# Performance work log

Measured on AMD Instinct MI355X. Metric: run time of the kernel, lower is better.

Reference implementation:

```python
import jax, jax.numpy as jnp
import numpy as np

GROUPS = 16
GROUP_SIZE = 16
K = 3
KK = K * K
BN_EPS = 1e-5


def setup_inputs() -> dict:
    key = jax.random.key(0)
    ks = jax.random.split(key, 6)
    B, C, H, W = 16, 256, 56, 56
    mid = C // 4  # rd_ratio = 4
    x = jax.random.normal(ks[0], (B, C, H, W), dtype=jnp.float32)
    w1 = jax.random.normal(ks[1], (mid, C), dtype=jnp.float32) * (1.0 / np.sqrt(C))
    bn_gamma = jnp.ones((mid,), dtype=jnp.float32)
    bn_beta = jnp.zeros((mid,), dtype=jnp.float32)
    bn_mean = jax.random.normal(ks[2], (mid,), dtype=jnp.float32) * 0.1
    bn_var = jax.random.uniform(ks[3], (mid,), dtype=jnp.float32, minval=0.5, maxval=1.5)
    w2 = jax.random.normal(ks[4], (KK * GROUPS, mid), dtype=jnp.float32) * (1.0 / np.sqrt(mid))
    b2 = jax.random.normal(ks[5], (KK * GROUPS,), dtype=jnp.float32) * 0.01
    return {"x": x, "w1": w1, "bn_gamma": bn_gamma, "bn_beta": bn_beta,
            "bn_mean": bn_mean, "bn_var": bn_var, "w2": w2, "b2": b2}


def reference(x, w1, bn_gamma, bn_beta, bn_mean, bn_var, w2, b2):
    B, C, H, W = x.shape
    # conv1: 1x1 conv + BatchNorm (eval) + ReLU
    t = jnp.einsum('bchw,oc->bohw', x, w1)
    scale = bn_gamma / jnp.sqrt(bn_var + BN_EPS)
    t = t * scale[None, :, None, None] + (bn_beta - bn_mean * scale)[None, :, None, None]
    t = jax.nn.relu(t)
    # conv2: 1x1 conv producing per-pixel kernels (B, KK*groups, H, W)
    weight = jnp.einsum('bchw,oc->bohw', t, w2) + b2[None, :, None, None]
    weight = weight.reshape(B, GROUPS, 1, KK, H, W)
    # unfold: extract 3x3 patches (pad=1, stride=1), kernel positions row-major
    xp = jnp.pad(x, ((0, 0), (0, 0), (1, 1), (1, 1)))
    patches = jnp.stack(
        [xp[:, :, i:i + H, j:j + W] for i in range(K) for j in range(K)],
        axis=2)  # (B, C, KK, H, W), matches torch unfold's (c*KK + kk) layout
    patches = patches.reshape(B, GROUPS, GROUP_SIZE, KK, H, W)
    out = (weight * patches).sum(axis=3).reshape(B, C, H, W)
    return out
```

## Files before the change

### kernel.cpp

```cpp
#include <hip/hip_runtime.h>


#define Cn    256
#define MID   64
#define Hn    56
#define Wn    56
#define HW    3136
#define Bn    16
#define NPIX  (Bn * HW)
#define CHW   (Cn * HW)
#define NKK   9
#define NG    16
#define GSZ   16
#define PXT   64
#define BN_EPS 1e-5f

#define GLOAD_LDS(src, dst, sz)                                                        \
  __builtin_amdgcn_global_load_lds(                                                    \
      (const __attribute__((address_space(1))) void*)(src),                            \
      (__attribute__((address_space(3))) void*)(dst), (sz), 0, 0)

__global__ __launch_bounds__(256) void prep_kernel(
    const float* __restrict__ w1,
    const float* __restrict__ gamma,
    const float* __restrict__ beta,
    const float* __restrict__ mean,
    const float* __restrict__ var,
    float* __restrict__ w1f,
    float* __restrict__ bias1) {
  int idx = blockIdx.x * 256 + threadIdx.x;
  if (idx < MID * Cn) {
    int c = idx >> 6;
    int o = idx & 63;
    float scale = gamma[o] / sqrtf(var[o] + BN_EPS);
    w1f[idx] = w1[o * Cn + c] * scale;
  } else if (idx < MID * Cn + MID) {
    int o = idx - MID * Cn;
    float scale = gamma[o] / sqrtf(var[o] + BN_EPS);
    bias1[o] = beta[o] - mean[o] * scale;
  }
}

__global__ __launch_bounds__(256) void fused_kernel(
    const float* __restrict__ x,
    const float* __restrict__ w1f,
    const float* __restrict__ bias1,
    const float* __restrict__ w2,
    const float* __restrict__ b2,
    float* __restrict__ out) {
  __shared__ float lt[MID][PXT];
  __shared__ __align__(16) float uni[9216];

  const int tid = threadIdx.x;
  const int px  = tid & 63;
  const int wvv = tid >> 6;
  const int wv  = __builtin_amdgcn_readfirstlane(wvv);

  const int px0 = blockIdx.x * PXT;
  const int b   = px0 / HW;
  const int hw0 = px0 - b * HW;
  const float* xb = x + (size_t)b * CHW + hw0;

  {
#pragma unroll
    for (int j = 0; j < 4; ++j) {
      const int c = (wv << 2) + j;
      GLOAD_LDS(xb + (size_t)c * HW + px, &uni[c * 64], 4);
    }
    GLOAD_LDS(w1f + (wv << 8) + (px << 2), &uni[2048 + (wv << 8)], 16);
  }
  __syncthreads();

  float acc[16];
#pragma unroll
  for (int j = 0; j < 16; ++j) acc[j] = 0.0f;

  for (int k = 0; k < 16; ++k) {
    const int cur = k & 1;
    if (k < 15) {
      const int nb = cur ^ 1;
      const int kb = k + 1;
#pragma unroll
      for (int j = 0; j < 4; ++j) {
        const int c = (wv << 2) + j;
        GLOAD_LDS(xb + (size_t)(kb * 16 + c) * HW + px, &uni[nb * 1024 + c * 64], 4);
      }
      GLOAD_LDS(w1f + kb * 1024 + (wv << 8) + (px << 2),
                &uni[2048 + nb * 1024 + (wv << 8)], 16);
    }
    const float* lx = &uni[cur * 1024];
    const float* lw = &uni[2048 + cur * 1024 + (wv << 4)];
#pragma unroll
    for (int c = 0; c < 16; ++c) {
      const float xv = lx[(c << 6) + px];
      const float4 w40 = *(const float4*)(lw + (c << 6) + 0);
      const float4 w41 = *(const float4*)(lw + (c << 6) + 4);
      const float4 w42 = *(const float4*)(lw + (c << 6) + 8);
      const float4 w43 = *(const float4*)(lw + (c << 6) + 12);
      acc[0]  = fmaf(xv, w40.x, acc[0]);
      acc[1]  = fmaf(xv, w40.y, acc[1]);
      acc[2]  = fmaf(xv, w40.z, acc[2]);
      acc[3]  = fmaf(xv, w40.w, acc[3]);
      acc[4]  = fmaf(xv, w41.x, acc[4]);
      acc[5]  = fmaf(xv, w41.y, acc[5]);
      acc[6]  = fmaf(xv, w41.z, acc[6]);
      acc[7]  = fmaf(xv, w41.w, acc[7]);
      acc[8]  = fmaf(xv, w42.x, acc[8]);
      acc[9]  = fmaf(xv, w42.y, acc[9]);
      acc[10] = fmaf(xv, w42.z, acc[10]);
      acc[11] = fmaf(xv, w42.w, acc[11]);
      acc[12] = fmaf(xv, w43.x, acc[12]);
      acc[13] = fmaf(xv, w43.y, acc[13]);
      acc[14] = fmaf(xv, w43.z, acc[14]);
      acc[15] = fmaf(xv, w43.w, acc[15]);
    }
    __syncthreads();
  }

#pragma unroll
  for (int j = 0; j < 16; ++j) {
    const int o = (wv << 4) + j;
    lt[o][px] = fmaxf(acc[j] + bias1[o], 0.0f);
  }
#pragma unroll
  for (int i = 0; i < 9; ++i) {
    const int r = wv * 9 + i;
    GLOAD_LDS(w2 + ((size_t)r << 8) + (px << 2), &uni[r << 8], 16);
  }
  __syncthreads();

  const int hw = hw0 + px;
  const int h  = hw / Wn;
  const int w  = hw - h * Wn;

  int off[NKK];
  unsigned vmask = 0;
#pragma unroll
  for (int kk = 0; kk < NKK; ++kk) {
    const int di  = kk / 3 - 1;
    const int dj  = kk % 3 - 1;
    const int h2  = h + di;
    const int w2v = w + dj;
    const bool valid = ((unsigned)h2 < (unsigned)Hn) && ((unsigned)w2v < (unsigned)Wn);
    off[kk] = valid ? (h2 * Wn + w2v) : hw;
    vmask |= (valid ? 1u : 0u) << kk;
  }

  const float* xg = x + (size_t)b * CHW;
  float* ob = out + (size_t)b * CHW + hw;

  for (int gi = 0; gi < 4; ++gi) {
    const int g = wv + (gi << 2);
    float a[NKK];
#pragma unroll
    for (int kk = 0; kk < NKK; ++kk) a[kk] = b2[g * NKK + kk];

#pragma unroll 4
    for (int o4 = 0; o4 < MID; o4 += 4) {
      const float t0 = lt[o4 + 0][px];
      const float t1 = lt[o4 + 1][px];
      const float t2 = lt[o4 + 2][px];
      const float t3 = lt[o4 + 3][px];
#pragma unroll
      for (int kk = 0; kk < NKK; ++kk) {
        const float4 w4 = *(const float4*)&uni[((g * NKK + kk) << 6) + o4];
        a[kk] = fmaf(t3, w4.w, fmaf(t2, w4.z, fmaf(t1, w4.y, fmaf(t0, w4.x, a[kk]))));
      }
    }

    float wk[NKK];
#pragma unroll
    for (int kk = 0; kk < NKK; ++kk)
      wk[kk] = ((vmask >> kk) & 1u) ? a[kk] : 0.0f;

    const float* xc0 = xg + (size_t)(g * GSZ) * HW;
#pragma unroll 4
    for (int cc = 0; cc < GSZ; ++cc) {
      const float* xc = xc0 + (size_t)cc * HW;
      float s = 0.0f;
#pragma unroll
      for (int kk = 0; kk < NKK; ++kk)
        s = fmaf(wk[kk], xc[off[kk]], s);
      ob[(size_t)(g * GSZ + cc) * HW] = s;
    }
  }
}

extern "C" void kernel_launch(void* const* d_in, const int* in_sizes, int n_in,
                              void* d_out, int out_size, void* d_ws, size_t ws_size,
                              hipStream_t stream) {
  const float* x     = (const float*)d_in[0];
  const float* w1    = (const float*)d_in[1];
  const float* gamma = (const float*)d_in[2];
  const float* beta  = (const float*)d_in[3];
  const float* mean  = (const float*)d_in[4];
  const float* var   = (const float*)d_in[5];
  const float* w2    = (const float*)d_in[6];
  const float* b2    = (const float*)d_in[7];
  float* out = (float*)d_out;

  char* ws = (char*)d_ws;
  float* w1f   = (float*)ws;
  float* bias1 = (float*)(ws + (size_t)MID * Cn * 4);

  prep_kernel<<<(MID * Cn + MID + 255) / 256, 256, 0, stream>>>(
      w1, gamma, beta, mean, var, w1f, bias1);
  fused_kernel<<<NPIX / PXT, 256, 0, stream>>>(x, w1f, bias1, w2, b2, out);
}
```

Baseline: 197.6 us.

## Split fused kernel into conv1 and per-group-quarter conv2/involution kernels

Result: faster. 176.4 us (-10.7%).

```diff
diff --git a/kernel.cpp b/kernel.cpp
--- a/kernel.cpp
+++ b/kernel.cpp
@@ -41,15 +41,12 @@
   }
 }
 
-__global__ __launch_bounds__(256) void fused_kernel(
+__global__ __launch_bounds__(256) void conv1_kernel(
     const float* __restrict__ x,
     const float* __restrict__ w1f,
     const float* __restrict__ bias1,
-    const float* __restrict__ w2,
-    const float* __restrict__ b2,
-    float* __restrict__ out) {
-  __shared__ float lt[MID][PXT];
-  __shared__ __align__(16) float uni[9216];
+    float* __restrict__ t) {
+  __shared__ __align__(16) float sb[4096];
 
   const int tid = threadIdx.x;
   const int px  = tid & 63;
@@ -61,14 +58,12 @@
   const int hw0 = px0 - b * HW;
   const float* xb = x + (size_t)b * CHW + hw0;
 
-  {
-#pragma unroll
-    for (int j = 0; j < 4; ++j) {
-      const int c = (wv << 2) + j;
-      GLOAD_LDS(xb + (size_t)c * HW + px, &uni[c * 64], 4);
-    }
-    GLOAD_LDS(w1f + (wv << 8) + (px << 2), &uni[2048 + (wv << 8)], 16);
-  }
+#pragma unroll
+  for (int j = 0; j < 4; ++j) {
+    const int c = (wv << 2) + j;
+    GLOAD_LDS(xb + (size_t)c * HW + px, &sb[c * 64], 4);
+  }
+  GLOAD_LDS(w1f + (wv << 8) + (px << 2), &sb[2048 + (wv << 8)], 16);
   __syncthreads();
 
   float acc[16];
@@ -83,13 +78,13 @@
 #pragma unroll
       for (int j = 0; j < 4; ++j) {
         const int c = (wv << 2) + j;
-        GLOAD_LDS(xb + (size_t)(kb * 16 + c) * HW + px, &uni[nb * 1024 + c * 64], 4);
+        GLOAD_LDS(xb + (size_t)(kb * 16 + c) * HW + px, &sb[nb * 1024 + c * 64], 4);
       }
       GLOAD_LDS(w1f + kb * 1024 + (wv << 8) + (px << 2),
-                &uni[2048 + nb * 1024 + (wv << 8)], 16);
+                &sb[2048 + nb * 1024 + (wv << 8)], 16);
     }
-    const float* lx = &uni[cur * 1024];
-    const float* lw = &uni[2048 + cur * 1024 + (wv << 4)];
+    const float* lx = &sb[cur * 1024];
+    const float* lw = &sb[2048 + cur * 1024 + (wv << 4)];
 #pragma unroll
     for (int c = 0; c < 16; ++c) {
       const float xv = lx[(c << 6) + px];
@@ -120,14 +115,60 @@
 #pragma unroll
   for (int j = 0; j < 16; ++j) {
     const int o = (wv << 4) + j;
-    lt[o][px] = fmaxf(acc[j] + bias1[o], 0.0f);
-  }
-#pragma unroll
-  for (int i = 0; i < 9; ++i) {
-    const int r = wv * 9 + i;
-    GLOAD_LDS(w2 + ((size_t)r << 8) + (px << 2), &uni[r << 8], 16);
+    t[(size_t)o * NPIX + px0 + px] = fmaxf(acc[j] + bias1[o], 0.0f);
+  }
+}
+
+__global__ __launch_bounds__(256) void conv2_inv_kernel(
+    const float* __restrict__ x,
+    const float* __restrict__ t,
+    const float* __restrict__ w2,
+    const float* __restrict__ b2,
+    float* __restrict__ out) {
+  __shared__ float lt[MID][PXT];
+  __shared__ __align__(16) float lw2f[4 * NKK * MID];
+
+  const int tid = threadIdx.x;
+  const int px  = tid & 63;
+  const int wvv = tid >> 6;
+  const int wv  = __builtin_amdgcn_readfirstlane(wvv);
+
+  const int bid = blockIdx.x;
+  const int pc  = bid >> 2;
+  const int gq  = bid & 3;
+  const int g   = (gq << 2) + wv;
+
+  const int px0 = pc * PXT;
+  const int b   = px0 / HW;
+  const int hw0 = px0 - b * HW;
+
+#pragma unroll
+  for (int j = 0; j < 16; ++j) {
+    const int o = (wv << 4) + j;
+    GLOAD_LDS(t + (size_t)o * NPIX + px0 + px, &lt[o][0], 4);
+  }
+  for (int ch = wv; ch < 9; ch += 4) {
+    GLOAD_LDS(w2 + (size_t)gq * (4 * NKK * MID) + (ch << 8) + (px << 2),
+              &lw2f[ch << 8], 16);
   }
   __syncthreads();
+
+  float a[NKK];
+#pragma unroll
+  for (int kk = 0; kk < NKK; ++kk) a[kk] = b2[g * NKK + kk];
+  const float* wq = &lw2f[wv * (NKK * MID)];
+#pragma unroll 4
+  for (int o4 = 0; o4 < MID; o4 += 4) {
+    const float t0 = lt[o4 + 0][px];
+    const float t1 = lt[o4 + 1][px];
+    const float t2 = lt[o4 + 2][px];
+    const float t3 = lt[o4 + 3][px];
+#pragma unroll
+    for (int kk = 0; kk < NKK; ++kk) {
+      const float4 w4 = *(const float4*)&wq[(kk << 6) + o4];
+      a[kk] = fmaf(t3, w4.w, fmaf(t2, w4.z, fmaf(t1, w4.y, fmaf(t0, w4.x, a[kk]))));
+    }
+  }
 
   const int hw = hw0 + px;
   const int h  = hw / Wn;
@@ -146,43 +187,26 @@
     vmask |= (valid ? 1u : 0u) << kk;
   }
 
-  const float* xg = x + (size_t)b * CHW;
-  float* ob = out + (size_t)b * CHW + hw;
-
-  for (int gi = 0; gi < 4; ++gi) {
-    const int g = wv + (gi << 2);
-    float a[NKK];
-#pragma unroll
-    for (int kk = 0; kk < NKK; ++kk) a[kk] = b2[g * NKK + kk];
-
+  float wk[NKK];
+#pragma unroll
+  for (int kk = 0; kk < NKK; ++kk)
+    wk[kk] = ((vmask >> kk) & 1u) ? a[kk] : 0.0f;
+
+  const float* xc = x + (size_t)b * CHW + (size_t)(g * GSZ) * HW;
+  float* ob = out + (size_t)b * CHW + (size_t)(g * GSZ) * HW + hw;
 #pragma unroll 4
-    for (int o4 = 0; o4 < MID; o4 += 4) {
-      const float t0 = lt[o4 + 0][px];
-      const float t1 = lt[o4 + 1][px];
-      const float t2 = lt[o4 + 2][px];
-      const float t3 = lt[o4 + 3][px];
-#pragma unroll
-      for (int kk = 0; kk < NKK; ++kk) {
-        const float4 w4 = *(const float4*)&uni[((g * NKK + kk) << 6) + o4];
-        a[kk] = fmaf(t3, w4.w, fmaf(t2, w4.z, fmaf(t1, w4.y, fmaf(t0, w4.x, a[kk]))));
-      }
-    }
-
-    float wk[NKK];
-#pragma unroll
-    for (int kk = 0; kk < NKK; ++kk)
-      wk[kk] = ((vmask >> kk) & 1u) ? a[kk] : 0.0f;
-
-    const float* xc0 = xg + (size_t)(g * GSZ) * HW;
-#pragma unroll 4
-    for (int cc = 0; cc < GSZ; ++cc) {
-      const float* xc = xc0 + (size_t)cc * HW;
-      float s = 0.0f;
-#pragma unroll
-      for (int kk = 0; kk < NKK; ++kk)
-        s = fmaf(wk[kk], xc[off[kk]], s);
-      ob[(size_t)(g * GSZ + cc) * HW] = s;
-    }
+  for (int cc = 0; cc < GSZ; ++cc) {
+    const float* xp = xc + (size_t)cc * HW;
+    float s0 = wk[0] * xp[off[0]];
+    float s1 = wk[1] * xp[off[1]];
+    float s2 = wk[2] * xp[off[2]];
+    s0 = fmaf(wk[3], xp[off[3]], s0);
+    s1 = fmaf(wk[4], xp[off[4]], s1);
+    s2 = fmaf(wk[5], xp[off[5]], s2);
+    s0 = fmaf(wk[6], xp[off[6]], s0);
+    s1 = fmaf(wk[7], xp[off[7]], s1);
+    s2 = fmaf(wk[8], xp[off[8]], s2);
+    ob[(size_t)cc * HW] = s0 + s1 + s2;
   }
 }
 
@@ -200,10 +224,12 @@
   float* out = (float*)d_out;
 
   char* ws = (char*)d_ws;
-  float* w1f   = (float*)ws;
-  float* bias1 = (float*)(ws + (size_t)MID * Cn * 4);
+  float* t     = (float*)ws;
+  float* w1f   = (float*)(ws + (size_t)MID * NPIX * 4);
+  float* bias1 = (float*)(ws + (size_t)MID * NPIX * 4 + (size_t)MID * Cn * 4);
 
   prep_kernel<<<(MID * Cn + MID + 255) / 256, 256, 0, stream>>>(
       w1, gamma, beta, mean, var, w1f, bias1);
-  fused_kernel<<<NPIX / PXT, 256, 0, stream>>>(x, w1f, bias1, w2, b2, out);
-}
+  conv1_kernel<<<NPIX / PXT, 256, 0, stream>>>(x, w1f, bias1, t);
+  conv2_inv_kernel<<<NPIX / PXT * 4, 256, 0, stream>>>(x, t, w2, b2, out);
+}
```
